# Kernel optimization log

Hardware: AMD Instinct MI355X
Metric: run time of the kernel (lower is better)

The kernel has to match this reference:

```python
import jax, jax.numpy as jnp
import numpy as np

N_NODES = 100000
N_EDGES = 1600000
N_GRAPHS = 256
F_IN = 54


def setup_inputs() -> dict:
    key = jax.random.key(0)
    ks = jax.random.split(key, 16)
    x = jax.random.normal(ks[0], (N_NODES, F_IN), dtype=jnp.float32)
    edge_index = jax.random.randint(ks[1], (2, N_EDGES), 0, N_NODES, dtype=jnp.int32)
    batch = jnp.sort(jax.random.randint(ks[2], (N_NODES,), 0, N_GRAPHS, dtype=jnp.int32))

    def lin(k, fi, fo):
        kw, kb = jax.random.split(k)
        lim = 1.0 / np.sqrt(fi)
        W = jax.random.uniform(kw, (fi, fo), minval=-lim, maxval=lim, dtype=jnp.float32)
        b = jax.random.uniform(kb, (fo,), minval=-lim, maxval=lim, dtype=jnp.float32)
        return W, b

    W1, b1 = lin(ks[3], 54, 54)
    W2, b2 = lin(ks[4], 54, 108)
    W3, b3 = lin(ks[5], 108, 216)
    Wf1, bf1 = lin(ks[6], 216, 1024)
    Wf2, bf2 = lin(ks[7], 1024, 128)
    return {"x": x, "edge_index": edge_index, "batch": batch,
            "W1": W1, "b1": b1, "W2": W2, "b2": b2, "W3": W3, "b3": b3,
            "Wf1": Wf1, "bf1": bf1, "Wf2": Wf2, "bf2": bf2}


def _gcn_norm(edge_index, n):
    # add self-loops, symmetric degree normalization (PyG GCNConv default)
    loop = jnp.arange(n, dtype=edge_index.dtype)
    row = jnp.concatenate([edge_index[0], loop])
    col = jnp.concatenate([edge_index[1], loop])
    deg = jax.ops.segment_sum(jnp.ones_like(col, dtype=jnp.float32), col, num_segments=n)
    dinv = jnp.where(deg > 0, jax.lax.rsqrt(deg), 0.0)
    norm = dinv[row] * dinv[col]
    return row, col, norm


def _gcn_conv(x, row, col, norm, W, b, n):
    h = x @ W                                  # [N, Fout]
    msg = h[row] * norm[:, None]               # [E+N, Fout] gather + scale
    out = jax.ops.segment_sum(msg, col, num_segments=n)  # scatter-add
    return out + b


def reference(x, edge_index, batch, W1, b1, W2, b2, W3, b3, Wf1, bf1, Wf2, bf2):
    n = x.shape[0]
    row, col, norm = _gcn_norm(edge_index, n)
    h = jax.nn.relu(_gcn_conv(x, row, col, norm, W1, b1, n))
    h = jax.nn.relu(_gcn_conv(h, row, col, norm, W2, b2, n))
    h = jax.nn.relu(_gcn_conv(h, row, col, norm, W3, b3, n))
    # global mean pool per graph
    sums = jax.ops.segment_sum(h, batch, num_segments=N_GRAPHS)
    cnts = jax.ops.segment_sum(jnp.ones((n,), jnp.float32), batch, num_segments=N_GRAPHS)
    pooled = sums / jnp.maximum(cnts, 1.0)[:, None]   # [G, 216]
    g = jax.nn.relu(pooled @ Wf1 + bf1)               # dropout = identity (eval)
    return g @ Wf2 + bf2                              # [G, 128]
```

## Files before the change

kernel.cpp:

```cpp
#include <hip/hip_runtime.h>


typedef _Float16 f16;
typedef _Float16 f16x2 __attribute__((ext_vector_type(2)));
typedef _Float16 f16x8 __attribute__((ext_vector_type(8)));
typedef float f32x4 __attribute__((ext_vector_type(4)));

static __host__ __device__ inline int cdiv(int a, int b) { return (a + b - 1) / b; }

constexpr int BSPAN = 512;
constexpr int EPB   = 4096;
constexpr int EPT   = EPB / 256;

template <int V>
__device__ __forceinline__ void vload(float* d, const float* s) {
    if constexpr (V == 1) { d[0] = s[0]; }
    else if constexpr (V == 2) { float2 t = *reinterpret_cast<const float2*>(s); d[0] = t.x; d[1] = t.y; }
    else { float4 t = *reinterpret_cast<const float4*>(s); d[0] = t.x; d[1] = t.y; d[2] = t.z; d[3] = t.w; }
}

__device__ __forceinline__ void wpack_one(const float* W, f16* Wb, int K, int F,
                                          int KT, int idx) {
    int j = idx & 7;
    int lane = (idx >> 3) & 63;
    int fi = idx >> 9;
    int kt = fi % KT;
    int nt = fi / KT;
    int k = kt * 32 + (lane >> 4) * 8 + j;
    int nn = nt * 16 + (lane & 15);
    Wb[idx] = (k < K && nn < F) ? (f16)W[k * F + nn] : (f16)0.f;
}
__global__ void k_wpack3(const float* __restrict__ W1, const float* __restrict__ W2,
                         const float* __restrict__ W3, f16* __restrict__ w1b,
                         f16* __restrict__ w2b, f16* __restrict__ w3b) {
    constexpr int T1 = 4 * 2 * 512;
    constexpr int T2 = 7 * 2 * 512;
    constexpr int T3 = 14 * 4 * 512;
    int idx = blockIdx.x * blockDim.x + threadIdx.x;
    if (idx < T1) wpack_one(W1, w1b, 54, 54, 2, idx);
    else if (idx < T1 + T2) wpack_one(W2, w2b, 54, 108, 2, idx - T1);
    else if (idx < T1 + T2 + T3) wpack_one(W3, w3b, 108, 216, 4, idx - T1 - T2);
}

__global__ void k_setup(float* psum, int nf, int* bktCnt, int* bktCur) {
    int i = blockIdx.x * blockDim.x + threadIdx.x;
    if (i < nf) psum[i] = 0.f;
    if (i < 256) { bktCnt[i] = 0; bktCur[i] = 0; }
}

__global__ __launch_bounds__(256) void k_bkt_hist(const int* __restrict__ col,
                                                  int* bktCnt, int e, int nb) {
    __shared__ int hist[256];
    int t = threadIdx.x;
    hist[t] = 0;
    __syncthreads();
    int base = blockIdx.x * EPB;
#pragma unroll
    for (int j = 0; j < EPT; j++) {
        int idx = base + j * 256 + t;
        if (idx < e) atomicAdd(&hist[col[idx] >> 9], 1);
    }
    __syncthreads();
    if (t < nb && hist[t] > 0) atomicAdd(&bktCnt[t], hist[t]);
}

__device__ __forceinline__ int scan256_ex(int* sbuf, int v, int t) {
    sbuf[t] = v;
    __syncthreads();
    for (int off = 1; off < 256; off <<= 1) {
        int x = sbuf[t];
        int y = (t >= off) ? sbuf[t - off] : 0;
        __syncthreads();
        sbuf[t] = x + y;
        __syncthreads();
    }
    return sbuf[t] - v;
}

__global__ __launch_bounds__(256) void k_bkt_part(const int* __restrict__ row,
                                                  const int* __restrict__ col,
                                                  const int* __restrict__ bktCnt,
                                                  int* bktCur, unsigned int* __restrict__ ebuf,
                                                  int e, int nb) {
    __shared__ int sbuf[256];
    __shared__ int hist[256];
    __shared__ int base[256];
    __shared__ int lcur[256];
    int t = threadIdx.x;
    int boff = scan256_ex(sbuf, (t < nb) ? bktCnt[t] : 0, t);
    hist[t] = 0; lcur[t] = 0;
    __syncthreads();
    int bs = blockIdx.x * EPB;
    unsigned int pk[EPT];
    int b[EPT];
#pragma unroll
    for (int j = 0; j < EPT; j++) {
        int idx = bs + j * 256 + t;
        if (idx < e) {
            int c = col[idx];
            pk[j] = ((unsigned int)(c & (BSPAN - 1)) << 17) | (unsigned int)row[idx];
            b[j] = c >> 9;
            atomicAdd(&hist[b[j]], 1);
        } else b[j] = -1;
    }
    __syncthreads();
    if (t < nb && hist[t] > 0) base[t] = boff + atomicAdd(&bktCur[t], hist[t]);
    __syncthreads();
#pragma unroll
    for (int j = 0; j < EPT; j++) {
        if (b[j] >= 0) {
            int lofs = atomicAdd(&lcur[b[j]], 1);
            ebuf[base[b[j]] + lofs] = pk[j];
        }
    }
}

__global__ __launch_bounds__(256) void k_bkt_build(const unsigned int* __restrict__ ebuf,
                                                   const int* __restrict__ bktCnt,
                                                   int* __restrict__ rowptr,
                                                   float* __restrict__ dinv,
                                                   int* __restrict__ eSrc,
                                                   int n, int nb) {
    __shared__ int sbuf[256];
    __shared__ int hist[BSPAN];
    __shared__ int cur[BSPAN];
    int t = threadIdx.x;
    int bkt = blockIdx.x;

    int boff_ex = scan256_ex(sbuf, (t < nb) ? bktCnt[t] : 0, t);
    __shared__ int boff_s, cnt_s;
    if (t == bkt) boff_s = boff_ex;
    if (t == 0) cnt_s = bktCnt[bkt];
    hist[t] = 0; hist[t + 256] = 0;
    __syncthreads();
    int es = boff_s, ee = boff_s + cnt_s;

    {
        int i = es + t;
        for (; i + 3 * 256 < ee; i += 4 * 256) {
            unsigned p0 = ebuf[i], p1 = ebuf[i + 256], p2 = ebuf[i + 512], p3 = ebuf[i + 768];
            atomicAdd(&hist[p0 >> 17], 1);
            atomicAdd(&hist[p1 >> 17], 1);
            atomicAdd(&hist[p2 >> 17], 1);
            atomicAdd(&hist[p3 >> 17], 1);
        }
        for (; i < ee; i += 256) atomicAdd(&hist[ebuf[i] >> 17], 1);
    }
    __syncthreads();

    int h0 = hist[2 * t], h1 = hist[2 * t + 1];
    __syncthreads();
    int ex = scan256_ex(sbuf, h0 + h1, t);
    int e0 = es + ex, e1 = e0 + h0;

    int node0 = bkt * BSPAN;
    int n0 = node0 + 2 * t, n1 = node0 + 2 * t + 1;
    if (n0 <= n) rowptr[n0] = e0;
    if (n1 <= n) rowptr[n1] = e1;
    if (n0 < n) dinv[n0] = rsqrtf((float)(h0 + 1));
    if (n1 < n) dinv[n1] = rsqrtf((float)(h1 + 1));
    cur[2 * t] = e0; cur[2 * t + 1] = e1;
    __syncthreads();

    {
        int i = es + t;
        for (; i + 3 * 256 < ee; i += 4 * 256) {
            unsigned p0 = ebuf[i], p1 = ebuf[i + 256], p2 = ebuf[i + 512], p3 = ebuf[i + 768];
            int s0 = atomicAdd(&cur[p0 >> 17], 1);
            int s1 = atomicAdd(&cur[p1 >> 17], 1);
            int s2 = atomicAdd(&cur[p2 >> 17], 1);
            int s3 = atomicAdd(&cur[p3 >> 17], 1);
            eSrc[s0] = (int)(p0 & 0x1FFFFu);
            eSrc[s1] = (int)(p1 & 0x1FFFFu);
            eSrc[s2] = (int)(p2 & 0x1FFFFu);
            eSrc[s3] = (int)(p3 & 0x1FFFFu);
        }
        for (; i < ee; i += 256) {
            unsigned int p = ebuf[i];
            int slot = atomicAdd(&cur[p >> 17], 1);
            eSrc[slot] = (int)(p & 0x1FFFFu);
        }
    }
}

template <int F, int RS>
__global__ void k_prescale(const float* __restrict__ x, const float* __restrict__ dinv,
                           f16* __restrict__ xs, int n) {
    constexpr int CH = F / 2;
    int idx = blockIdx.x * blockDim.x + threadIdx.x;
    if (idx >= n * CH) return;
    int node = idx / CH;
    int c = idx - node * CH;
    float d = dinv[node];
    float v[2];
    vload<2>(v, x + (long long)node * F + c * 2);
    f16x2 h;
    h[0] = (f16)(v[0] * d);
    h[1] = (f16)(v[1] * d);
    *reinterpret_cast<f16x2*>(xs + (long long)node * RS + c * 2) = h;
}

__global__ void k_find_start(const int* __restrict__ batch, int* start, int n, int g) {
    int i = blockIdx.x * blockDim.x + threadIdx.x;
    if (i >= n) return;
    int b = batch[i];
    int bp = (i == 0) ? -1 : batch[i - 1];
    for (int gg = bp + 1; gg <= b; gg++) start[gg] = i;
    if (i == n - 1)
        for (int gg = b + 1; gg <= g; gg++) start[gg] = n;
}

template <int F, int KTILES, int NTILES, int FOUT, int OSTR, bool POOL>
__global__ __launch_bounds__(256) void k_gcn_fused(
        const int* __restrict__ rowptr, const int* __restrict__ eSrc,
        const float* __restrict__ dinv, const f16* __restrict__ hs,
        const f16* __restrict__ Wb, const float* __restrict__ bias,
        const int* __restrict__ batch, f16* __restrict__ outh,
        float* __restrict__ psum, int n) {
    constexpr int KPAD = KTILES * 32;
    constexpr int KP   = KPAD + 8;
    constexpr int CGN  = KPAD / 8;
    constexpr int EPW  = 64 / CGN;
    constexpr int NSLOT = 4;

    __shared__ __align__(16) f16 a_lds[64 * KP];
    __shared__ float psum_l[POOL ? NSLOT * FOUT : 1];

    int t = threadIdx.x;
    int node0 = blockIdx.x * 64;
    int w = t >> 6;
    int lane = t & 63;
    int eslot = lane / CGN;
    int cg = lane & (CGN - 1);
    int ch0 = cg * 8;
    int lim = F - ch0;
    if (lim > 8) lim = 8;
    if (lim < 0) lim = 0;

    if (POOL) {
        for (int i = t; i < NSLOT * FOUT; i += 256) psum_l[i] = 0.f;
    }

    const f16x8* src = reinterpret_cast<const f16x8*>(hs);

    for (int i = 0; i < 16; i++) {
        int node = node0 + w * 16 + i;
        float acc[8];
#pragma unroll
        for (int j = 0; j < 8; j++) acc[j] = 0.f;
        float di = 0.f;

        if (node < n) {
            int rs_ = rowptr[node], re = rowptr[node + 1];
            int deg = re - rs_;
            int myidx = 0;
            if (lane < deg) myidx = eSrc[rs_ + lane];

            if (eslot == 0) {
                f16x8 v = src[(long long)node * CGN + cg];
#pragma unroll
                for (int j = 0; j < 8; j++) acc[j] += (float)v[j];
            }

            int nfull = deg < 64 ? deg : 64;
            int base = 0;
            for (; base + 4 * EPW <= nfull; base += 4 * EPW) {
                int s0 = __shfl(myidx, base + eslot);
                int s1 = __shfl(myidx, base + EPW + eslot);
                int s2 = __shfl(myidx, base + 2 * EPW + eslot);
                int s3 = __shfl(myidx, base + 3 * EPW + eslot);
                f16x8 v0 = src[(long long)s0 * CGN + cg];
                f16x8 v1 = src[(long long)s1 * CGN + cg];
                f16x8 v2 = src[(long long)s2 * CGN + cg];
                f16x8 v3 = src[(long long)s3 * CGN + cg];
#pragma unroll
                for (int j = 0; j < 8; j++)
                    acc[j] += ((float)v0[j] + (float)v1[j]) + ((float)v2[j] + (float)v3[j]);
            }
            for (; base + 2 * EPW <= nfull; base += 2 * EPW) {
                int s0 = __shfl(myidx, base + eslot);
                int s1 = __shfl(myidx, base + EPW + eslot);
                f16x8 v0 = src[(long long)s0 * CGN + cg];
                f16x8 v1 = src[(long long)s1 * CGN + cg];
#pragma unroll
                for (int j = 0; j < 8; j++) acc[j] += (float)v0[j] + (float)v1[j];
            }
            for (; base + EPW <= nfull; base += EPW) {
                int s = __shfl(myidx, base + eslot);
                f16x8 v = src[(long long)s * CGN + cg];
#pragma unroll
                for (int j = 0; j < 8; j++) acc[j] += (float)v[j];
            }
            if (base < nfull) {
                int idx = base + eslot;
                int s = __shfl(myidx, idx < 63 ? idx : 63);
                if (idx < nfull) {
                    f16x8 v = src[(long long)s * CGN + cg];
#pragma unroll
                    for (int j = 0; j < 8; j++) acc[j] += (float)v[j];
                }
            }
            for (int e = rs_ + 64 + eslot; e < re; e += EPW) {
                int s = eSrc[e];
                f16x8 v = src[(long long)s * CGN + cg];
#pragma unroll
                for (int j = 0; j < 8; j++) acc[j] += (float)v[j];
            }

#pragma unroll
            for (int j = 0; j < 8; j++)
                if (j >= lim) acc[j] = 0.f;
#pragma unroll
            for (int m = CGN; m < 64; m <<= 1)
#pragma unroll
                for (int j = 0; j < 8; j++) acc[j] += __shfl_xor(acc[j], m);

            di = dinv[node];
        }

        if (eslot == 0) {
            f16x8 o;
#pragma unroll
            for (int j = 0; j < 8; j++) o[j] = (f16)(acc[j] * di);
            *reinterpret_cast<f16x8*>(&a_lds[(w * 16 + i) * KP + ch0]) = o;
        }
    }
    __syncthreads();

    int quad = lane >> 4;
    int col = lane & 15;

    f16x8 afr[KTILES];
#pragma unroll
    for (int kt = 0; kt < KTILES; kt++)
        afr[kt] = *reinterpret_cast<const f16x8*>(
            &a_lds[(16 * w + col) * KP + kt * 32 + quad * 8]);

    int nodeC = node0 + 16 * w + quad * 4;
    float dv[4];
    int gb[4];
#pragma unroll
    for (int r = 0; r < 4; r++) {
        int nd = nodeC + r;
        bool valid = nd < n;
        if (POOL) {
            gb[r] = valid ? batch[nd] : -1;
            dv[r] = 0.f;
        } else {
            dv[r] = valid ? dinv[nd] : 0.f;
            gb[r] = -1;
        }
    }
    int g0 = POOL ? batch[node0] : 0;

    const f16x8* wb = reinterpret_cast<const f16x8*>(Wb);
#pragma unroll
    for (int nt = 0; nt < NTILES; nt++) {
        f16x8 bfr[KTILES];
#pragma unroll
        for (int kt = 0; kt < KTILES; kt++)
            bfr[kt] = wb[(nt * KTILES + kt) * 64 + lane];
        f32x4 acc = {0.f, 0.f, 0.f, 0.f};
#pragma unroll
        for (int kt = 0; kt < KTILES; kt++)
            acc = __builtin_amdgcn_mfma_f32_16x16x32_f16(afr[kt], bfr[kt], acc, 0, 0, 0);

        int ch = nt * 16 + col;
        if (ch < FOUT) {
            float bval = bias[ch];
            if (POOL) {
                if (gb[0] == gb[3] && gb[0] >= 0) {
                    float s = fmaxf(acc[0] + bval, 0.f) + fmaxf(acc[1] + bval, 0.f)
                            + fmaxf(acc[2] + bval, 0.f) + fmaxf(acc[3] + bval, 0.f);
                    int slot = gb[0] - g0;
                    if (slot < NSLOT) atomicAdd(&psum_l[slot * FOUT + ch], s);
                    else atomicAdd(&psum[gb[0] * FOUT + ch], s);
                } else {
#pragma unroll
                    for (int r = 0; r < 4; r++) {
                        if (gb[r] < 0) continue;
                        float v = fmaxf(acc[r] + bval, 0.f);
                        int slot = gb[r] - g0;
                        if (slot < NSLOT) atomicAdd(&psum_l[slot * FOUT + ch], v);
                        else atomicAdd(&psum[gb[r] * FOUT + ch], v);
                    }
                }
            } else {
#pragma unroll
                for (int r = 0; r < 4; r++) {
                    int nd = nodeC + r;
                    if (nd < n)
                        outh[(long long)nd * OSTR + ch] =
                            (f16)(fmaxf(acc[r] + bval, 0.f) * dv[r]);
                }
            }
        }
    }

    if (POOL) {
        __syncthreads();
        int lastNode = node0 + 63;
        if (lastNode >= n) lastNode = n - 1;
        int nsl = batch[lastNode] - g0 + 1;
        if (nsl > NSLOT) nsl = NSLOT;
        for (int f = t; f < nsl * FOUT; f += 256) {
            float v = psum_l[f];
            if (v != 0.f) atomicAdd(&psum[(g0 + f / FOUT) * FOUT + (f % FOUT)], v);
        }
    }
}

__global__ void k_fc1(const float* __restrict__ P, const int* __restrict__ start,
                      const float* __restrict__ W, const float* __restrict__ bias,
                      float* __restrict__ out) {
    int row = blockIdx.x >> 2;
    int o = (blockIdx.x & 3) * 256 + threadIdx.x;
    int cnt = start[row + 1] - start[row];
    float scale = 1.0f / fmaxf((float)cnt, 1.0f);
    __shared__ float prow[216];
    if (threadIdx.x < 216) prow[threadIdx.x] = P[row * 216 + threadIdx.x] * scale;
    __syncthreads();
    float acc = bias[o];
    for (int k = 0; k < 216; k++) acc += prow[k] * W[k * 1024 + o];
    out[row * 1024 + o] = fmaxf(acc, 0.f);
}
__global__ void k_fc2(const float* __restrict__ G, const float* __restrict__ W,
                      const float* __restrict__ bias, float* __restrict__ out) {
    int row = blockIdx.x;
    int o = threadIdx.x;
    __shared__ float grow[1024];
    for (int k = threadIdx.x; k < 1024; k += 128) grow[k] = G[row * 1024 + k];
    __syncthreads();
    float acc = bias[o];
    for (int k = 0; k < 1024; k++) acc += grow[k] * W[k * 128 + o];
    out[row * 128 + o] = acc;
}

extern "C" void kernel_launch(void* const* d_in, const int* in_sizes, int n_in,
                              void* d_out, int out_size, void* d_ws, size_t ws_size,
                              hipStream_t stream) {
    const float* x     = (const float*)d_in[0];
    const int*   ei    = (const int*)d_in[1];
    const int*   batch = (const int*)d_in[2];
    const float* W1  = (const float*)d_in[3];
    const float* b1  = (const float*)d_in[4];
    const float* W2  = (const float*)d_in[5];
    const float* b2  = (const float*)d_in[6];
    const float* W3  = (const float*)d_in[7];
    const float* b3  = (const float*)d_in[8];
    const float* Wf1 = (const float*)d_in[9];
    const float* bf1 = (const float*)d_in[10];
    const float* Wf2 = (const float*)d_in[11];
    const float* bf2 = (const float*)d_in[12];
    float* out = (float*)d_out;

    const int N = in_sizes[0] / 54;
    const int E = in_sizes[1] / 2;
    const int G = 256;
    const int* row = ei;
    const int* col = ei + E;
    const int NB = cdiv(N, BSPAN);
    const int NBLK_A = cdiv(E, EPB);

    char* ws = (char*)d_ws;
    size_t off = 0;
    auto carve = [&](size_t bytes) {
        void* p = ws + off;
        off += (bytes + 255) & ~(size_t)255;
        return p;
    };
    int*   rowptr  = (int*)carve((size_t)(N + 1) * 4);
    int*   bktCnt  = (int*)carve(256 * 4);
    int*   bktCur  = (int*)carve(256 * 4);
    int*   eSrc    = (int*)carve((size_t)E * 4);
    float* dinv    = (float*)carve((size_t)N * 4);
    f16*   xs      = (f16*)carve((size_t)N * 64 * 2);
    f16*   hsbuf   = (f16*)carve((size_t)N * 128 * 2);
    f16*   bufA    = (f16*)carve((size_t)N * 128 * 2);
    unsigned int* ebuf = (unsigned int*)carve((size_t)E * 4);
    float* psum    = (float*)carve((size_t)G * 216 * 4);
    float* gbuf    = (float*)carve((size_t)G * 1024 * 4);
    int*   start   = (int*)carve((size_t)(G + 1) * 4);
    f16*   w1b     = (f16*)carve((size_t)4 * 2 * 512 * 2);
    f16*   w2b     = (f16*)carve((size_t)7 * 2 * 512 * 2);
    f16*   w3b     = (f16*)carve((size_t)14 * 4 * 512 * 2);

    const int T = 256;

    k_setup<<<cdiv(G * 216, T), T, 0, stream>>>(psum, G * 216, bktCnt, bktCur);
    k_wpack3<<<cdiv((4 * 2 + 7 * 2 + 14 * 4) * 512, T), T, 0, stream>>>(
        W1, W2, W3, w1b, w2b, w3b);
    k_find_start<<<cdiv(N, T), T, 0, stream>>>(batch, start, N, G);

    k_bkt_hist<<<NBLK_A, 256, 0, stream>>>(col, bktCnt, E, NB);
    k_bkt_part<<<NBLK_A, 256, 0, stream>>>(row, col, bktCnt, bktCur, ebuf, E, NB);
    k_bkt_build<<<NB, 256, 0, stream>>>(ebuf, bktCnt, rowptr, dinv, eSrc, N, NB);

    k_prescale<54, 64><<<cdiv(N * 27, T), T, 0, stream>>>(x, dinv, xs, N);

    const int GB = cdiv(N, 64);

    k_gcn_fused<54, 2, 4, 54, 64, false><<<GB, 256, 0, stream>>>(
        rowptr, eSrc, dinv, xs, w1b, b1, nullptr, hsbuf, nullptr, N);

    k_gcn_fused<54, 2, 7, 108, 128, false><<<GB, 256, 0, stream>>>(
        rowptr, eSrc, dinv, hsbuf, w2b, b2, nullptr, bufA, nullptr, N);

    k_gcn_fused<108, 4, 14, 216, 0, true><<<GB, 256, 0, stream>>>(
        rowptr, eSrc, dinv, bufA, w3b, b3, batch, nullptr, psum, N);

    k_fc1<<<G * 4, T, 0, stream>>>(psum, start, Wf1, bf1, gbuf);
    k_fc2<<<G, 128, 0, stream>>>(gbuf, Wf2, bf2, out);
}
```

Before: 405.2 us.

## Split layer-3 into per-node gather kernel and separate GEMM+pool kernel

Layer 3's fused gather+MFMA+pool kernel is replaced by two kernels. The first is a one-wave-per-node gather that writes the aggregated features to a buffer. The second is an MFMA GEMM that reads them from that buffer and does the mean-pool atomics. This is meant to give the heavy 108-wide gather more parallelism and latency hiding, instead of 16 serial nodes per wave. It costs an extra global write and read of the N×128 half intermediate. Three small init kernels are also merged into one launch.

```diff
diff --git a/kernel.cpp b/kernel.cpp
--- a/kernel.cpp
+++ b/kernel.cpp
@@ -30,22 +30,30 @@
     int nn = nt * 16 + (lane & 15);
     Wb[idx] = (k < K && nn < F) ? (f16)W[k * F + nn] : (f16)0.f;
 }
-__global__ void k_wpack3(const float* __restrict__ W1, const float* __restrict__ W2,
-                         const float* __restrict__ W3, f16* __restrict__ w1b,
-                         f16* __restrict__ w2b, f16* __restrict__ w3b) {
+
+__global__ void k_init(const int* __restrict__ batch, int* __restrict__ start,
+                       float* __restrict__ psum, int* __restrict__ bktCnt,
+                       int* __restrict__ bktCur,
+                       const float* __restrict__ W1, const float* __restrict__ W2,
+                       const float* __restrict__ W3, f16* __restrict__ w1b,
+                       f16* __restrict__ w2b, f16* __restrict__ w3b,
+                       int n, int g) {
+    int i = blockIdx.x * blockDim.x + threadIdx.x;
+    if (i < g * 216) psum[i] = 0.f;
+    if (i < 256) { bktCnt[i] = 0; bktCur[i] = 0; }
     constexpr int T1 = 4 * 2 * 512;
     constexpr int T2 = 7 * 2 * 512;
     constexpr int T3 = 14 * 4 * 512;
-    int idx = blockIdx.x * blockDim.x + threadIdx.x;
-    if (idx < T1) wpack_one(W1, w1b, 54, 54, 2, idx);
-    else if (idx < T1 + T2) wpack_one(W2, w2b, 54, 108, 2, idx - T1);
-    else if (idx < T1 + T2 + T3) wpack_one(W3, w3b, 108, 216, 4, idx - T1 - T2);
-}
-
-__global__ void k_setup(float* psum, int nf, int* bktCnt, int* bktCur) {
-    int i = blockIdx.x * blockDim.x + threadIdx.x;
-    if (i < nf) psum[i] = 0.f;
-    if (i < 256) { bktCnt[i] = 0; bktCur[i] = 0; }
+    if (i < T1) wpack_one(W1, w1b, 54, 54, 2, i);
+    else if (i < T1 + T2) wpack_one(W2, w2b, 54, 108, 2, i - T1);
+    else if (i < T1 + T2 + T3) wpack_one(W3, w3b, 108, 216, 4, i - T1 - T2);
+    if (i < n) {
+        int b = batch[i];
+        int bp = (i == 0) ? -1 : batch[i - 1];
+        for (int gg = bp + 1; gg <= b; gg++) start[gg] = i;
+        if (i == n - 1)
+            for (int gg = b + 1; gg <= g; gg++) start[gg] = n;
+    }
 }
 
 __global__ __launch_bounds__(256) void k_bkt_hist(const int* __restrict__ col,
@@ -200,31 +208,114 @@
     *reinterpret_cast<f16x2*>(xs + (long long)node * RS + c * 2) = h;
 }
 
-__global__ void k_find_start(const int* __restrict__ batch, int* start, int n, int g) {
-    int i = blockIdx.x * blockDim.x + threadIdx.x;
-    if (i >= n) return;
-    int b = batch[i];
-    int bp = (i == 0) ? -1 : batch[i - 1];
-    for (int gg = bp + 1; gg <= b; gg++) start[gg] = i;
-    if (i == n - 1)
-        for (int gg = b + 1; gg <= g; gg++) start[gg] = n;
-}
-
-template <int F, int KTILES, int NTILES, int FOUT, int OSTR, bool POOL>
+template <int F, int RS>
+__global__ __launch_bounds__(256) void k_gatherw(
+        const int* __restrict__ rowptr, const int* __restrict__ eSrc,
+        const float* __restrict__ dinv, const f16* __restrict__ hs,
+        f16* __restrict__ out, int n) {
+    constexpr int CGN = RS / 8;
+    constexpr int EPW = 64 / CGN;
+    int wave = threadIdx.x >> 6;
+    int lane = threadIdx.x & 63;
+    int eslot = lane / CGN;
+    int cg = lane & (CGN - 1);
+    int node = blockIdx.x * 4 + wave;
+    if (node >= n) return;
+    int ch0 = cg * 8;
+    int lim = F - ch0;
+    if (lim > 8) lim = 8;
+    if (lim < 0) lim = 0;
+
+    int rs_ = rowptr[node], re = rowptr[node + 1];
+    float di = dinv[node];
+    int deg = re - rs_;
+    int myidx = 0;
+    if (lane < deg) myidx = eSrc[rs_ + lane];
+
+    const f16x8* src = reinterpret_cast<const f16x8*>(hs);
+    float acc[8];
+#pragma unroll
+    for (int j = 0; j < 8; j++) acc[j] = 0.f;
+
+    if (eslot == 0) {
+        f16x8 v = src[(long long)node * CGN + cg];
+#pragma unroll
+        for (int j = 0; j < 8; j++) acc[j] += (float)v[j];
+    }
+
+    int nfull = deg < 64 ? deg : 64;
+    int base = 0;
+    for (; base + 4 * EPW <= nfull; base += 4 * EPW) {
+        int s0 = __shfl(myidx, base + eslot);
+        int s1 = __shfl(myidx, base + EPW + eslot);
+        int s2 = __shfl(myidx, base + 2 * EPW + eslot);
+        int s3 = __shfl(myidx, base + 3 * EPW + eslot);
+        f16x8 v0 = src[(long long)s0 * CGN + cg];
+        f16x8 v1 = src[(long long)s1 * CGN + cg];
+        f16x8 v2 = src[(long long)s2 * CGN + cg];
+        f16x8 v3 = src[(long long)s3 * CGN + cg];
+#pragma unroll
+        for (int j = 0; j < 8; j++)
+            acc[j] += ((float)v0[j] + (float)v1[j]) + ((float)v2[j] + (float)v3[j]);
+    }
+    for (; base + 2 * EPW <= nfull; base += 2 * EPW) {
+        int s0 = __shfl(myidx, base + eslot);
+        int s1 = __shfl(myidx, base + EPW + eslot);
+        f16x8 v0 = src[(long long)s0 * CGN + cg];
+        f16x8 v1 = src[(long long)s1 * CGN + cg];
+#pragma unroll
+        for (int j = 0; j < 8; j++) acc[j] += (float)v0[j] + (float)v1[j];
+    }
+    for (; base + EPW <= nfull; base += EPW) {
+        int s = __shfl(myidx, base + eslot);
+        f16x8 v = src[(long long)s * CGN + cg];
+#pragma unroll
+        for (int j = 0; j < 8; j++) acc[j] += (float)v[j];
+    }
+    if (base < nfull) {
+        int idx = base + eslot;
+        int s = __shfl(myidx, idx < 63 ? idx : 63);
+        if (idx < nfull) {
+            f16x8 v = src[(long long)s * CGN + cg];
+#pragma unroll
+            for (int j = 0; j < 8; j++) acc[j] += (float)v[j];
+        }
+    }
+    for (int e = rs_ + 64 + eslot; e < re; e += EPW) {
+        int s = eSrc[e];
+        f16x8 v = src[(long long)s * CGN + cg];
+#pragma unroll
+        for (int j = 0; j < 8; j++) acc[j] += (float)v[j];
+    }
+
+#pragma unroll
+    for (int j = 0; j < 8; j++)
+        if (j >= lim) acc[j] = 0.f;
+#pragma unroll
+    for (int m = CGN; m < 64; m <<= 1)
+#pragma unroll
+        for (int j = 0; j < 8; j++) acc[j] += __shfl_xor(acc[j], m);
+
+    if (eslot == 0) {
+        f16x8 o;
+#pragma unroll
+        for (int j = 0; j < 8; j++) o[j] = (f16)(acc[j] * di);
+        *reinterpret_cast<f16x8*>(out + (long long)node * RS + ch0) = o;
+    }
+}
+
+template <int F, int KTILES, int NTILES, int FOUT, int OSTR>
 __global__ __launch_bounds__(256) void k_gcn_fused(
         const int* __restrict__ rowptr, const int* __restrict__ eSrc,
         const float* __restrict__ dinv, const f16* __restrict__ hs,
         const f16* __restrict__ Wb, const float* __restrict__ bias,
-        const int* __restrict__ batch, f16* __restrict__ outh,
-        float* __restrict__ psum, int n) {
+        f16* __restrict__ outh, int n) {
     constexpr int KPAD = KTILES * 32;
     constexpr int KP   = KPAD + 8;
     constexpr int CGN  = KPAD / 8;
     constexpr int EPW  = 64 / CGN;
-    constexpr int NSLOT = 4;
 
     __shared__ __align__(16) f16 a_lds[64 * KP];
-    __shared__ float psum_l[POOL ? NSLOT * FOUT : 1];
 
     int t = threadIdx.x;
     int node0 = blockIdx.x * 64;
@@ -237,10 +328,6 @@
     if (lim > 8) lim = 8;
     if (lim < 0) lim = 0;
 
-    if (POOL) {
-        for (int i = t; i < NSLOT * FOUT; i += 256) psum_l[i] = 0.f;
-    }
-
     const f16x8* src = reinterpret_cast<const f16x8*>(hs);
 
     for (int i = 0; i < 16; i++) {
@@ -252,6 +339,7 @@
 
         if (node < n) {
             int rs_ = rowptr[node], re = rowptr[node + 1];
+            di = dinv[node];
             int deg = re - rs_;
             int myidx = 0;
             if (lane < deg) myidx = eSrc[rs_ + lane];
@@ -314,8 +402,6 @@
             for (int m = CGN; m < 64; m <<= 1)
 #pragma unroll
                 for (int j = 0; j < 8; j++) acc[j] += __shfl_xor(acc[j], m);
-
-            di = dinv[node];
         }
 
         if (eslot == 0) {
@@ -338,20 +424,11 @@
 
     int nodeC = node0 + 16 * w + quad * 4;
     float dv[4];
-    int gb[4];
 #pragma unroll
     for (int r = 0; r < 4; r++) {
         int nd = nodeC + r;
-        bool valid = nd < n;
-        if (POOL) {
-            gb[r] = valid ? batch[nd] : -1;
-            dv[r] = 0.f;
-        } else {
-            dv[r] = valid ? dinv[nd] : 0.f;
-            gb[r] = -1;
-        }
-    }
-    int g0 = POOL ? batch[node0] : 0;
+        dv[r] = (nd < n) ? dinv[nd] : 0.f;
+    }
 
     const f16x8* wb = reinterpret_cast<const f16x8*>(Wb);
 #pragma unroll
@@ -368,45 +445,106 @@
         int ch = nt * 16 + col;
         if (ch < FOUT) {
             float bval = bias[ch];
-            if (POOL) {
-                if (gb[0] == gb[3] && gb[0] >= 0) {
-                    float s = fmaxf(acc[0] + bval, 0.f) + fmaxf(acc[1] + bval, 0.f)
-                            + fmaxf(acc[2] + bval, 0.f) + fmaxf(acc[3] + bval, 0.f);
-                    int slot = gb[0] - g0;
-                    if (slot < NSLOT) atomicAdd(&psum_l[slot * FOUT + ch], s);
-                    else atomicAdd(&psum[gb[0] * FOUT + ch], s);
-                } else {
-#pragma unroll
-                    for (int r = 0; r < 4; r++) {
-                        if (gb[r] < 0) continue;
-                        float v = fmaxf(acc[r] + bval, 0.f);
-                        int slot = gb[r] - g0;
-                        if (slot < NSLOT) atomicAdd(&psum_l[slot * FOUT + ch], v);
-                        else atomicAdd(&psum[gb[r] * FOUT + ch], v);
-                    }
+#pragma unroll
+            for (int r = 0; r < 4; r++) {
+                int nd = nodeC + r;
+                if (nd < n)
+                    outh[(long long)nd * OSTR + ch] =
+                        (f16)(fmaxf(acc[r] + bval, 0.f) * dv[r]);
+            }
+        }
+    }
+}
+
+template <int KTILES, int NTILES, int K, int FOUT>
+__global__ __launch_bounds__(256) void k_gemm_pool(
+        const f16* __restrict__ in, const f16* __restrict__ Wb,
+        const float* __restrict__ bias, const int* __restrict__ batch,
+        float* __restrict__ psum, int n) {
+    constexpr int KPAD = KTILES * 32;
+    constexpr int KP   = KPAD + 8;
+    constexpr int V8   = KPAD / 8;
+    constexpr int NSLOT = 4;
+
+    __shared__ f16 a_lds[64 * KP];
+    __shared__ float psum_l[NSLOT * FOUT];
+
+    int t = threadIdx.x;
+    int node0 = blockIdx.x * 64;
+
+    const f16x8* inp = reinterpret_cast<const f16x8*>(in);
+    for (int f = t; f < 64 * V8; f += 256) {
+        int node = f / V8;
+        int v = f - node * V8;
+        f16x8 val = {};
+        if (node0 + node < n) val = inp[(long long)(node0 + node) * V8 + v];
+        *reinterpret_cast<f16x8*>(&a_lds[node * KP + v * 8]) = val;
+    }
+    for (int i = t; i < NSLOT * FOUT; i += 256) psum_l[i] = 0.f;
+    __syncthreads();
+
+    int w = t >> 6;
+    int lane = t & 63;
+    int quad = lane >> 4;
+    int col = lane & 15;
+
+    f16x8 afr[KTILES];
+#pragma unroll
+    for (int kt = 0; kt < KTILES; kt++)
+        afr[kt] = *reinterpret_cast<const f16x8*>(
+            &a_lds[(16 * w + col) * KP + kt * 32 + quad * 8]);
+
+    int nodeC = node0 + 16 * w + quad * 4;
+    int gb[4];
+#pragma unroll
+    for (int r = 0; r < 4; r++) {
+        int nd = nodeC + r;
+        gb[r] = (nd < n) ? batch[nd] : -1;
+    }
+    int g0 = batch[node0];
+
+    const f16x8* wb = reinterpret_cast<const f16x8*>(Wb);
+#pragma unroll
+    for (int nt = 0; nt < NTILES; nt++) {
+        f16x8 bfr[KTILES];
+#pragma unroll
+        for (int kt = 0; kt < KTILES; kt++)
+            bfr[kt] = wb[(nt * KTILES + kt) * 64 + lane];
+        f32x4 acc = {0.f, 0.f, 0.f, 0.f};
+#pragma unroll
+        for (int kt = 0; kt < KTILES; kt++)
+            acc = __builtin_amdgcn_mfma_f32_16x16x32_f16(afr[kt], bfr[kt], acc, 0, 0, 0);
+
+        int ch = nt * 16 + col;
+        if (ch < FOUT) {
+            float bval = bias[ch];
+            if (gb[0] == gb[3] && gb[0] >= 0) {
+                float s = fmaxf(acc[0] + bval, 0.f) + fmaxf(acc[1] + bval, 0.f)
+                        + fmaxf(acc[2] + bval, 0.f) + fmaxf(acc[3] + bval, 0.f);
+                int slot = gb[0] - g0;
+                if (slot < NSLOT) atomicAdd(&psum_l[slot * FOUT + ch], s);
+                else atomicAdd(&psum[gb[0] * FOUT + ch], s);
+            } else {
+#pragma unroll
+                for (int r = 0; r < 4; r++) {
+                    if (gb[r] < 0) continue;
+                    float v = fmaxf(acc[r] + bval, 0.f);
+                    int slot = gb[r] - g0;
+                    if (slot < NSLOT) atomicAdd(&psum_l[slot * FOUT + ch], v);
+                    else atomicAdd(&psum[gb[r] * FOUT + ch], v);
                 }
-            } else {
-#pragma unroll
-                for (int r = 0; r < 4; r++) {
-                    int nd = nodeC + r;
-                    if (nd < n)
-                        outh[(long long)nd * OSTR + ch] =
-                            (f16)(fmaxf(acc[r] + bval, 0.f) * dv[r]);
-                }
-            }
-        }
-    }
-
-    if (POOL) {
-        __syncthreads();
-        int lastNode = node0 + 63;
-        if (lastNode >= n) lastNode = n - 1;
-        int nsl = batch[lastNode] - g0 + 1;
-        if (nsl > NSLOT) nsl = NSLOT;
-        for (int f = t; f < nsl * FOUT; f += 256) {
-            float v = psum_l[f];
-            if (v != 0.f) atomicAdd(&psum[(g0 + f / FOUT) * FOUT + (f % FOUT)], v);
-        }
+            }
+        }
+    }
+
+    __syncthreads();
+    int lastNode = node0 + 63;
+    if (lastNode >= n) lastNode = n - 1;
+    int nsl = batch[lastNode] - g0 + 1;
+    if (nsl > NSLOT) nsl = NSLOT;
+    for (int f = t; f < nsl * FOUT; f += 256) {
+        float v = psum_l[f];
+        if (v != 0.f) atomicAdd(&psum[(g0 + f / FOUT) * FOUT + (f % FOUT)], v);
     }
 }
 
@@ -487,10 +625,8 @@
 
     const int T = 256;
 
-    k_setup<<<cdiv(G * 216, T), T, 0, stream>>>(psum, G * 216, bktCnt, bktCur);
-    k_wpack3<<<cdiv((4 * 2 + 7 * 2 + 14 * 4) * 512, T), T, 0, stream>>>(
-        W1, W2, W3, w1b, w2b, w3b);
-    k_find_start<<<cdiv(N, T), T, 0, stream>>>(batch, start, N, G);
+    k_init<<<cdiv(N, T), T, 0, stream>>>(batch, start, psum, bktCnt, bktCur,
+                                         W1, W2, W3, w1b, w2b, w3b, N, G);
 
     k_bkt_hist<<<NBLK_A, 256, 0, stream>>>(col, bktCnt, E, NB);
     k_bkt_part<<<NBLK_A, 256, 0, stream>>>(row, col, bktCnt, bktCur, ebuf, E, NB);
@@ -500,14 +636,15 @@
 
     const int GB = cdiv(N, 64);
 
-    k_gcn_fused<54, 2, 4, 54, 64, false><<<GB, 256, 0, stream>>>(
-        rowptr, eSrc, dinv, xs, w1b, b1, nullptr, hsbuf, nullptr, N);
-
-    k_gcn_fused<54, 2, 7, 108, 128, false><<<GB, 256, 0, stream>>>(
-        rowptr, eSrc, dinv, hsbuf, w2b, b2, nullptr, bufA, nullptr, N);
-
-    k_gcn_fused<108, 4, 14, 216, 0, true><<<GB, 256, 0, stream>>>(
-        rowptr, eSrc, dinv, bufA, w3b, b3, batch, nullptr, psum, N);
+    k_gcn_fused<54, 2, 4, 54, 64><<<GB, 256, 0, stream>>>(
+        rowptr, eSrc, dinv, xs, w1b, b1, hsbuf, N);
+
+    k_gcn_fused<54, 2, 7, 108, 128><<<GB, 256, 0, stream>>>(
+        rowptr, eSrc, dinv, hsbuf, w2b, b2, bufA, N);
+
+    k_gatherw<108, 128><<<cdiv(N, 4), 256, 0, stream>>>(rowptr, eSrc, dinv, bufA, hsbuf, N);
+    k_gemm_pool<4, 14, 108, 216><<<GB, 256, 0, stream>>>(
+        hsbuf, w3b, b3, batch, psum, N);
 
     k_fc1<<<G * 4, T, 0, stream>>>(psum, start, Wf1, bf1, gbuf);
     k_fc2<<<G, 128, 0, stream>>>(gbuf, Wf2, bf2, out);
```

Measured after the change: 388.0 us. -4.2%, faster.
